# Kernel optimization log

Measured on AMD Instinct MI355X. Metric: run time of the kernel, lower is better.

The kernel has to match this reference:

```python
import jax, jax.numpy as jnp
import numpy as np

N_NODES = 100000
N_EDGES = 1600000
IN_DIM = 256
OUT_DIM = 128
SELF_LOOP_W = 2.0  # improved=True


def setup_inputs() -> dict:
    key = jax.random.key(0)
    ks = jax.random.split(key, 9)
    x = jax.random.normal(ks[0], (N_NODES, IN_DIM), dtype=jnp.float32)
    edge_index = jax.random.randint(ks[1], (2, N_EDGES), 0, N_NODES, dtype=jnp.int64)
    edge_weight = jax.random.uniform(ks[2], (N_EDGES,), dtype=jnp.float32)
    s1 = 1.0 / np.sqrt(IN_DIM)
    s2 = 1.0 / np.sqrt(OUT_DIM)
    W1 = jax.random.normal(ks[3], (IN_DIM, OUT_DIM), dtype=jnp.float32) * s1
    b1 = jnp.zeros((OUT_DIM,), dtype=jnp.float32)
    W_mu = jax.random.normal(ks[4], (OUT_DIM, OUT_DIM), dtype=jnp.float32) * s2
    b_mu = jnp.zeros((OUT_DIM,), dtype=jnp.float32)
    W_var = jax.random.normal(ks[5], (OUT_DIM, OUT_DIM), dtype=jnp.float32) * s2
    b_var = jnp.zeros((OUT_DIM,), dtype=jnp.float32)
    return {"x": x, "edge_index": edge_index, "edge_weight": edge_weight,
            "W1": W1, "b1": b1, "W_mu": W_mu, "b_mu": b_mu,
            "W_var": W_var, "b_var": b_var}


def _gcn_norm(edge_index, edge_weight, num_nodes):
    # add self loops with fill value 2.0 (improved=True), then symmetric norm
    loop = jnp.arange(num_nodes, dtype=edge_index.dtype)
    row = jnp.concatenate([edge_index[0], loop])
    col = jnp.concatenate([edge_index[1], loop])
    ew = jnp.concatenate([edge_weight,
                          jnp.full((num_nodes,), SELF_LOOP_W, dtype=edge_weight.dtype)])
    deg = jax.ops.segment_sum(ew, col, num_segments=num_nodes)
    dis = jnp.where(deg > 0, jax.lax.rsqrt(jnp.where(deg > 0, deg, 1.0)), 0.0)
    norm = dis[row] * ew * dis[col]
    return row, col, norm


def _gcn_conv(x, row, col, norm, W, b, num_nodes):
    xw = x @ W                      # [N, out]
    msg = xw[row] * norm[:, None]   # [E+N, out] per-edge messages
    out = jax.ops.segment_sum(msg, col, num_segments=num_nodes)
    return out + b


def reference(x, edge_index, edge_weight, W1, b1, W_mu, b_mu, W_var, b_var):
    n = x.shape[0]
    row, col, norm = _gcn_norm(edge_index, edge_weight, n)
    feat = jax.nn.relu(_gcn_conv(x, row, col, norm, W1, b1, n))
    mu = _gcn_conv(feat, row, col, norm, W_mu, b_mu, n)
    var = _gcn_conv(feat, row, col, norm, W_var, b_var, n)
    return (mu, var)
```

## Files before the change

### kernel.cpp

```cpp
#include <hip/hip_runtime.h>
#include <hip/hip_bf16.h>

#define CDIV(a,b) (((a)+(b)-1)/(b))

typedef __attribute__((ext_vector_type(8))) short short8;
typedef __attribute__((ext_vector_type(4))) float f32x4;

static __device__ inline short f2bf(float f) {
    union { __hip_bfloat16 h; short s; } u;
    u.h = __float2bfloat16(f);
    return u.s;
}
static __device__ inline ushort f2bfu(float f) { return (ushort)f2bf(f); }
static __device__ inline float bfu_lo(uint v) { return __uint_as_float(v << 16); }
static __device__ inline float bfu_hi(uint v) { return __uint_as_float(v & 0xffff0000u); }


__global__ __launch_bounds__(512) void k_init(unsigned long long* __restrict__ pack, int n,
                                              const float* __restrict__ W1,
                                              short* __restrict__ W1t,
                                              const float* __restrict__ Wmu,
                                              const float* __restrict__ Wvar,
                                              short* __restrict__ Wcat) {
    int i = blockIdx.x * 512 + threadIdx.x;
    if (i < n) pack[i] = 0ull;
    if (i < 128 * 256) {
        int k = i % 256, col = i / 256;
        W1t[i] = f2bf(W1[(size_t)k * 128 + col]);
    } else if (i < 2 * 128 * 256) {
        int j = i - 128 * 256;
        int k = j & 127, col = j >> 7;
        float v = (col < 128) ? Wmu[(size_t)k * 128 + col] : Wvar[(size_t)k * 128 + (col - 128)];
        Wcat[j] = f2bf(v);
    }
}


__global__ __launch_bounds__(512) void k_fat(const float* __restrict__ A,
                                             const short* __restrict__ Bt,
                                             ushort* __restrict__ C, int n, int nGB,
                                             const int* __restrict__ col,
                                             const float* __restrict__ ew,
                                             unsigned long long* __restrict__ pack,
                                             int* __restrict__ rank, int E) {
    const int K = 256;
    __shared__ short Blds[128 * K];
    int t = threadIdx.x;

    if (blockIdx.x >= nGB) {
        int e = (blockIdx.x - nGB) * 512 + t;
        if (e < E) {
            int c = col[e];
            unsigned long long q = (unsigned long long)(ew[e] * 16777216.0f + 0.5f);
            unsigned long long old = atomicAdd(&pack[c], (1ull << 40) | q);
            rank[e] = (int)(old >> 40);
        }
        return;
    }

    const int CHK = K / 8;
    for (int c = t; c < 128 * CHK; c += 512) {
        int colw = c / CHK;
        int kb  = (c % CHK) * 16;
        int dst = colw * (K * 2) + (kb ^ ((colw & 7) << 4));
        *(float4*)((char*)Blds + dst) =
            *(const float4*)((const char*)Bt + (size_t)colw * (K * 2) + kb);
    }
    __syncthreads();

    int wave = t >> 6, lane = t & 63;
    int lg = lane >> 4, lr = lane & 15;
    long row_base = (long)blockIdx.x * 256 + wave * 32;

    long ra0 = row_base + lr;      if (ra0 > n - 1) ra0 = n - 1;
    long ra1 = row_base + 16 + lr; if (ra1 > n - 1) ra1 = n - 1;

    f32x4 acc[2][8];
    #pragma unroll
    for (int i = 0; i < 2; ++i)
        #pragma unroll
        for (int j = 0; j < 8; ++j) acc[i][j] = (f32x4){0.f, 0.f, 0.f, 0.f};

    const float* pa0 = A + ra0 * K + lg * 8;
    const float* pa1 = A + ra1 * K + lg * 8;

    for (int k0 = 0; k0 < K; k0 += 32) {
        float4 x0 = *(const float4*)(pa0 + k0);
        float4 x1 = *(const float4*)(pa0 + k0 + 4);
        float4 y0 = *(const float4*)(pa1 + k0);
        float4 y1 = *(const float4*)(pa1 + k0 + 4);
        short8 a0, a1;
        a0[0]=f2bf(x0.x); a0[1]=f2bf(x0.y); a0[2]=f2bf(x0.z); a0[3]=f2bf(x0.w);
        a0[4]=f2bf(x1.x); a0[5]=f2bf(x1.y); a0[6]=f2bf(x1.z); a0[7]=f2bf(x1.w);
        a1[0]=f2bf(y0.x); a1[1]=f2bf(y0.y); a1[2]=f2bf(y0.z); a1[3]=f2bf(y0.w);
        a1[4]=f2bf(y1.x); a1[5]=f2bf(y1.y); a1[6]=f2bf(y1.z); a1[7]=f2bf(y1.w);

        int kb = (k0 + lg * 8) * 2;
        #pragma unroll
        for (int cb = 0; cb < 8; ++cb) {
            int colm = cb * 16 + lr;
            short8 b = *(short8*)((char*)Blds + colm * (K * 2) + (kb ^ ((colm & 7) << 4)));
            acc[0][cb] = __builtin_amdgcn_mfma_f32_16x16x32_bf16(a0, b, acc[0][cb], 0, 0, 0);
            acc[1][cb] = __builtin_amdgcn_mfma_f32_16x16x32_bf16(a1, b, acc[1][cb], 0, 0, 0);
        }
    }

    #pragma unroll
    for (int rf = 0; rf < 2; ++rf) {
        #pragma unroll
        for (int cb = 0; cb < 8; ++cb) {
            int colm = cb * 16 + lr;
            #pragma unroll
            for (int r = 0; r < 4; ++r) {
                long row = row_base + rf * 16 + lg * 4 + r;
                if (row < n) C[row * 128 + colm] = f2bfu(acc[rf][cb][r]);
            }
        }
    }
}


__global__ __launch_bounds__(256) void k_scan1(const unsigned long long* __restrict__ pack,
                                               float* __restrict__ dis,
                                               int* __restrict__ row_ptr,
                                               int* __restrict__ bsum, int n) {
    int t = threadIdx.x;
    int base = blockIdx.x * 1024 + t * 4;
    int v0 = 0, v1 = 0, v2 = 0, v3 = 0;
    #pragma unroll
    for (int j = 0; j < 4; ++j) {
        int idx = base + j;
        if (idx < n) {
            unsigned long long p = pack[idx];
            float deg = 2.0f + (float)(p & ((1ull << 40) - 1)) * (1.0f / 16777216.0f);
            dis[idx] = rsqrtf(deg);
            int c = (int)(p >> 40);
            if (j == 0) v0 = c; else if (j == 1) v1 = c; else if (j == 2) v2 = c; else v3 = c;
        }
    }
    int tsum = v0 + v1 + v2 + v3;
    int lane = t & 63, wv = t >> 6;
    int val = tsum;
    #pragma unroll
    for (int d = 1; d < 64; d <<= 1) {
        int u = __shfl_up(val, d, 64);
        if (lane >= d) val += u;
    }
    __shared__ int ws[4];
    if (lane == 63) ws[wv] = val;
    __syncthreads();
    int woff = 0;
    #pragma unroll
    for (int i = 0; i < 4; ++i) if (i < wv) woff += ws[i];
    int excl = woff + val - tsum;
    if (base + 0 < n) row_ptr[base + 0] = excl;  excl += v0;
    if (base + 1 < n) row_ptr[base + 1] = excl;  excl += v1;
    if (base + 2 < n) row_ptr[base + 2] = excl;  excl += v2;
    if (base + 3 < n) row_ptr[base + 3] = excl;
    if (t == 255) bsum[blockIdx.x] = woff + val;
}

__global__ __launch_bounds__(128) void k_scan2(int* bsum, int nb, int* row_ptr, int n, int E) {
    int t = threadIdx.x;
    int v = (t < nb) ? bsum[t] : 0;
    int lane = t & 63, wv = t >> 6;
    int val = v;
    #pragma unroll
    for (int d = 1; d < 64; d <<= 1) {
        int u = __shfl_up(val, d, 64);
        if (lane >= d) val += u;
    }
    __shared__ int ws[2];
    if (lane == 63) ws[wv] = val;
    __syncthreads();
    int woff = (wv == 1) ? ws[0] : 0;
    if (t < nb) bsum[t] = woff + val - v;
    if (t == 0) row_ptr[n] = E;
}

__global__ __launch_bounds__(256) void k_scan3(int* __restrict__ row_ptr,
                                               const int* __restrict__ bsum, int n) {
    int i = blockIdx.x * 256 + threadIdx.x;
    if (i < n) row_ptr[i] += bsum[i >> 10];
}

__global__ __launch_bounds__(512) void k_fill(const int* __restrict__ rowi,
                                              const int* __restrict__ coli,
                                              const float* __restrict__ ew,
                                              const int* __restrict__ rank,
                                              const float* __restrict__ dis,
                                              const int* __restrict__ row_ptr,
                                              int2* __restrict__ csr, int E) {
    int e = blockIdx.x * 512 + threadIdx.x;
    if (e < E) {
        int c = coli[e], r = rowi[e];
        int pos = row_ptr[c] + rank[e];
        csr[pos] = make_int2(r, __float_as_int(dis[r] * ew[e]));
    }
}


template<int OUTMODE>
__global__ __launch_bounds__(256) void k_agg(const uint* __restrict__ src,
                                             const int* __restrict__ row_ptr,
                                             const int2* __restrict__ csr,
                                             const float* __restrict__ dis,
                                             const float* __restrict__ bias,
                                             uint* __restrict__ dst, int n) {
    int wid = (blockIdx.x * 256 + threadIdx.x) >> 6;
    int lane = threadIdx.x & 63;
    if (wid >= n) return;
    int e0 = row_ptr[wid], e1 = row_ptr[wid + 1];

    float a0=0.f,b0=0.f,a1=0.f,b1=0.f,a2=0.f,b2=0.f,a3=0.f,b3=0.f;
    float a4=0.f,b4=0.f,a5=0.f,b5=0.f,a6=0.f,b6=0.f,a7=0.f,b7=0.f;
    int e = e0;
    for (; e + 7 < e1; e += 8) {
        int2 c0 = csr[e],     c1 = csr[e + 1], c2 = csr[e + 2], c3 = csr[e + 3];
        int2 c4 = csr[e + 4], c5 = csr[e + 5], c6 = csr[e + 6], c7 = csr[e + 7];
        uint v0 = src[(size_t)c0.x * 64 + lane];
        uint v1 = src[(size_t)c1.x * 64 + lane];
        uint v2 = src[(size_t)c2.x * 64 + lane];
        uint v3 = src[(size_t)c3.x * 64 + lane];
        uint v4 = src[(size_t)c4.x * 64 + lane];
        uint v5 = src[(size_t)c5.x * 64 + lane];
        uint v6 = src[(size_t)c6.x * 64 + lane];
        uint v7 = src[(size_t)c7.x * 64 + lane];
        float w0 = __int_as_float(c0.y), w1 = __int_as_float(c1.y);
        float w2 = __int_as_float(c2.y), w3 = __int_as_float(c3.y);
        float w4 = __int_as_float(c4.y), w5 = __int_as_float(c5.y);
        float w6 = __int_as_float(c6.y), w7 = __int_as_float(c7.y);
        a0 += w0 * bfu_lo(v0); b0 += w0 * bfu_hi(v0);
        a1 += w1 * bfu_lo(v1); b1 += w1 * bfu_hi(v1);
        a2 += w2 * bfu_lo(v2); b2 += w2 * bfu_hi(v2);
        a3 += w3 * bfu_lo(v3); b3 += w3 * bfu_hi(v3);
        a4 += w4 * bfu_lo(v4); b4 += w4 * bfu_hi(v4);
        a5 += w5 * bfu_lo(v5); b5 += w5 * bfu_hi(v5);
        a6 += w6 * bfu_lo(v6); b6 += w6 * bfu_hi(v6);
        a7 += w7 * bfu_lo(v7); b7 += w7 * bfu_hi(v7);
    }
    for (; e + 1 < e1; e += 2) {
        int2 c0 = csr[e], c1 = csr[e + 1];
        uint v0 = src[(size_t)c0.x * 64 + lane];
        uint v1 = src[(size_t)c1.x * 64 + lane];
        float w0 = __int_as_float(c0.y), w1 = __int_as_float(c1.y);
        a0 += w0 * bfu_lo(v0); b0 += w0 * bfu_hi(v0);
        a1 += w1 * bfu_lo(v1); b1 += w1 * bfu_hi(v1);
    }
    if (e < e1) {
        int2 c = csr[e];
        uint v = src[(size_t)c.x * 64 + lane];
        float w = __int_as_float(c.y);
        a0 += w * bfu_lo(v); b0 += w * bfu_hi(v);
    }
    float dc = dis[wid];
    uint sv = src[(size_t)wid * 64 + lane];
    float sw = 2.f * dc * dc;
    float ox = dc * (((a0 + a1) + (a2 + a3)) + ((a4 + a5) + (a6 + a7))) + sw * bfu_lo(sv);
    float oy = dc * (((b0 + b1) + (b2 + b3)) + ((b4 + b5) + (b6 + b7))) + sw * bfu_hi(sv);
    if constexpr (OUTMODE == 0) {
        ox += bias[lane * 2]; oy += bias[lane * 2 + 1];
        ox = fmaxf(ox, 0.f);  oy = fmaxf(oy, 0.f);
    }
    dst[(size_t)wid * 64 + lane] = (uint)f2bfu(ox) | ((uint)f2bfu(oy) << 16);
}


__global__ __launch_bounds__(512) void k_gemm2(const short* __restrict__ A,
                                               const short* __restrict__ Bt,
                                               const float* __restrict__ bmu,
                                               const float* __restrict__ bvar,
                                               float* __restrict__ out,
                                               int n) {
    const int K = 128;
    __shared__ short Blds[256 * K];
    int t = threadIdx.x;

    const int CHK = K / 8;
    for (int c = t; c < 256 * CHK; c += 512) {
        int col = c / CHK;
        int kb  = (c % CHK) * 16;
        int dst = col * (K * 2) + (kb ^ ((col & 7) << 4));
        *(float4*)((char*)Blds + dst) =
            *(const float4*)((const char*)Bt + (size_t)col * (K * 2) + kb);
    }
    __syncthreads();

    int wave = t >> 6, lane = t & 63;
    int lg = lane >> 4, lr = lane & 15;
    int colbase = (wave & 1) * 128;
    long row_base = (long)blockIdx.x * 128 + (wave >> 1) * 32;

    long ra0 = row_base + lr;      if (ra0 > n - 1) ra0 = n - 1;
    long ra1 = row_base + 16 + lr; if (ra1 > n - 1) ra1 = n - 1;

    f32x4 acc[2][8];
    #pragma unroll
    for (int i = 0; i < 2; ++i)
        #pragma unroll
        for (int j = 0; j < 8; ++j) acc[i][j] = (f32x4){0.f, 0.f, 0.f, 0.f};

    const short* pa0 = A + ra0 * K + lg * 8;
    const short* pa1 = A + ra1 * K + lg * 8;

    #pragma unroll
    for (int k0 = 0; k0 < K; k0 += 32) {
        short8 a0 = *(const short8*)(pa0 + k0);
        short8 a1 = *(const short8*)(pa1 + k0);
        int kb = (k0 + lg * 8) * 2;
        #pragma unroll
        for (int cb = 0; cb < 8; ++cb) {
            int col = colbase + cb * 16 + lr;
            short8 b = *(short8*)((char*)Blds + col * (K * 2) + (kb ^ ((col & 7) << 4)));
            acc[0][cb] = __builtin_amdgcn_mfma_f32_16x16x32_bf16(a0, b, acc[0][cb], 0, 0, 0);
            acc[1][cb] = __builtin_amdgcn_mfma_f32_16x16x32_bf16(a1, b, acc[1][cb], 0, 0, 0);
        }
    }

    #pragma unroll
    for (int rf = 0; rf < 2; ++rf) {
        #pragma unroll
        for (int cb = 0; cb < 8; ++cb) {
            int colc = colbase + cb * 16 + lr;
            bool is_var = colc >= 128;
            int col = is_var ? colc - 128 : colc;
            float bv = is_var ? bvar[col] : bmu[col];
            size_t obase = is_var ? (size_t)n * 128 : 0;
            #pragma unroll
            for (int r = 0; r < 4; ++r) {
                long row = row_base + rf * 16 + lg * 4 + r;
                if (row < n)
                    __builtin_nontemporal_store(acc[rf][cb][r] + bv,
                                                &out[obase + (size_t)row * 128 + col]);
            }
        }
    }
}


extern "C" void kernel_launch(void* const* d_in, const int* in_sizes, int n_in,
                              void* d_out, int out_size, void* d_ws, size_t ws_size,
                              hipStream_t stream) {
    const float* x    = (const float*)d_in[0];
    const int*   ei   = (const int*)d_in[1];
    const float* ew   = (const float*)d_in[2];
    const float* W1   = (const float*)d_in[3];
    const float* b1   = (const float*)d_in[4];
    const float* Wmu  = (const float*)d_in[5];
    const float* bmu  = (const float*)d_in[6];
    const float* Wvar = (const float*)d_in[7];
    const float* bvar = (const float*)d_in[8];

    const int E = in_sizes[2];
    const int N = in_sizes[0] / 256;
    const int* rowi = ei;
    const int* coli = ei + E;

    char* base = (char*)d_ws;
    size_t off = 0;
    auto alloc = [&](size_t bytes) -> void* {
        void* p = base + off;
        off = (off + bytes + 511) & ~(size_t)511;
        return p;
    };
    unsigned long long* pack = (unsigned long long*)alloc((size_t)N * 8);
    float* dis     = (float*)alloc((size_t)N * 4);
    int*   row_ptr = (int*)  alloc((size_t)(N + 1) * 4);
    int*   rank    = (int*)  alloc((size_t)E * 4);
    int*   bsum    = (int*)  alloc(1024 * 4);
    int2*  csr     = (int2*) alloc((size_t)E * 8);
    uint*  xw      = (uint*) alloc((size_t)N * 64 * 4);
    uint*  feat    = (uint*) alloc((size_t)N * 64 * 4);
    short* W1t     = (short*)alloc((size_t)256 * 128 * 2);
    short* Wcat    = (short*)alloc((size_t)256 * 128 * 2);
    uint*  g       = xw;

    int nb   = CDIV(N, 1024);
    int nGB  = CDIV(N, 256);
    int nCB  = CDIV(E, 512);

    k_init<<<CDIV(N, 512), 512, 0, stream>>>(pack, N, W1, W1t, Wmu, Wvar, Wcat);

    k_fat<<<nGB + nCB, 512, 0, stream>>>(x, W1t, (ushort*)xw, N, nGB, coli, ew, pack, rank, E);

    k_scan1<<<nb, 256, 0, stream>>>(pack, dis, row_ptr, bsum, N);
    k_scan2<<<1, 128, 0, stream>>>(bsum, nb, row_ptr, N, E);
    k_scan3<<<CDIV(N, 256), 256, 0, stream>>>(row_ptr, bsum, N);
    k_fill <<<CDIV(E, 512), 512, 0, stream>>>(rowi, coli, ew, rank, dis, row_ptr, csr, E);

    k_agg<0><<<CDIV(N * 64, 256), 256, 0, stream>>>(xw, row_ptr, csr, dis, b1, feat, N);
    k_agg<1><<<CDIV(N * 64, 256), 256, 0, stream>>>(feat, row_ptr, csr, dis, nullptr, g, N);
    k_gemm2<<<CDIV(N, 128), 512, 0, stream>>>((const short*)g, Wcat, bmu, bvar, (float*)d_out, N);
}
```

Before: 305.7 us.

## Halve k_fat LDS via two-phase K staging; split agg wave into edge halves

The first GEMM kernel now stages the 256-wide weight matrix in shared memory as two 128-wide halves. This halves its LDS footprint so more blocks can reside per CU, at the cost of an extra barrier and reload. The aggregation kernel now splits each wave into two 32-lane halves that each handle alternate edges with 8-byte vector loads of a full feature row. The halves are combined with a cross-half shuffle, which gives more gathers in flight per wave, and only half the lanes write the output.

```diff
diff --git a/kernel.cpp b/kernel.cpp
--- a/kernel.cpp
+++ b/kernel.cpp
@@ -43,8 +43,8 @@
                                              const float* __restrict__ ew,
                                              unsigned long long* __restrict__ pack,
                                              int* __restrict__ rank, int E) {
-    const int K = 256;
-    __shared__ short Blds[128 * K];
+    const int K = 256, KH = 128;
+    __shared__ short Blds[128 * KH];
     int t = threadIdx.x;
 
     if (blockIdx.x >= nGB) {
@@ -58,16 +58,6 @@
         return;
     }
 
-    const int CHK = K / 8;
-    for (int c = t; c < 128 * CHK; c += 512) {
-        int colw = c / CHK;
-        int kb  = (c % CHK) * 16;
-        int dst = colw * (K * 2) + (kb ^ ((colw & 7) << 4));
-        *(float4*)((char*)Blds + dst) =
-            *(const float4*)((const char*)Bt + (size_t)colw * (K * 2) + kb);
-    }
-    __syncthreads();
-
     int wave = t >> 6, lane = t & 63;
     int lg = lane >> 4, lr = lane & 15;
     long row_base = (long)blockIdx.x * 256 + wave * 32;
@@ -84,24 +74,39 @@
     const float* pa0 = A + ra0 * K + lg * 8;
     const float* pa1 = A + ra1 * K + lg * 8;
 
-    for (int k0 = 0; k0 < K; k0 += 32) {
-        float4 x0 = *(const float4*)(pa0 + k0);
-        float4 x1 = *(const float4*)(pa0 + k0 + 4);
-        float4 y0 = *(const float4*)(pa1 + k0);
-        float4 y1 = *(const float4*)(pa1 + k0 + 4);
-        short8 a0, a1;
-        a0[0]=f2bf(x0.x); a0[1]=f2bf(x0.y); a0[2]=f2bf(x0.z); a0[3]=f2bf(x0.w);
-        a0[4]=f2bf(x1.x); a0[5]=f2bf(x1.y); a0[6]=f2bf(x1.z); a0[7]=f2bf(x1.w);
-        a1[0]=f2bf(y0.x); a1[1]=f2bf(y0.y); a1[2]=f2bf(y0.z); a1[3]=f2bf(y0.w);
-        a1[4]=f2bf(y1.x); a1[5]=f2bf(y1.y); a1[6]=f2bf(y1.z); a1[7]=f2bf(y1.w);
-
-        int kb = (k0 + lg * 8) * 2;
-        #pragma unroll
-        for (int cb = 0; cb < 8; ++cb) {
-            int colm = cb * 16 + lr;
-            short8 b = *(short8*)((char*)Blds + colm * (K * 2) + (kb ^ ((colm & 7) << 4)));
-            acc[0][cb] = __builtin_amdgcn_mfma_f32_16x16x32_bf16(a0, b, acc[0][cb], 0, 0, 0);
-            acc[1][cb] = __builtin_amdgcn_mfma_f32_16x16x32_bf16(a1, b, acc[1][cb], 0, 0, 0);
+    #pragma unroll
+    for (int p = 0; p < 2; ++p) {
+        if (p) __syncthreads();
+        const int CHK = KH / 8;
+        for (int c = t; c < 128 * CHK; c += 512) {
+            int colw = c / CHK;
+            int kb  = (c % CHK) * 16;
+            int dst = colw * (KH * 2) + (kb ^ ((colw & 7) << 4));
+            *(float4*)((char*)Blds + dst) =
+                *(const float4*)((const char*)Bt + (size_t)colw * (K * 2) + p * (KH * 2) + kb);
+        }
+        __syncthreads();
+
+        for (int k0 = 0; k0 < KH; k0 += 32) {
+            int kg = p * KH + k0;
+            float4 x0 = *(const float4*)(pa0 + kg);
+            float4 x1 = *(const float4*)(pa0 + kg + 4);
+            float4 y0 = *(const float4*)(pa1 + kg);
+            float4 y1 = *(const float4*)(pa1 + kg + 4);
+            short8 a0, a1;
+            a0[0]=f2bf(x0.x); a0[1]=f2bf(x0.y); a0[2]=f2bf(x0.z); a0[3]=f2bf(x0.w);
+            a0[4]=f2bf(x1.x); a0[5]=f2bf(x1.y); a0[6]=f2bf(x1.z); a0[7]=f2bf(x1.w);
+            a1[0]=f2bf(y0.x); a1[1]=f2bf(y0.y); a1[2]=f2bf(y0.z); a1[3]=f2bf(y0.w);
+            a1[4]=f2bf(y1.x); a1[5]=f2bf(y1.y); a1[6]=f2bf(y1.z); a1[7]=f2bf(y1.w);
+
+            int kb = (k0 + lg * 8) * 2;
+            #pragma unroll
+            for (int cb = 0; cb < 8; ++cb) {
+                int colm = cb * 16 + lr;
+                short8 b = *(short8*)((char*)Blds + colm * (KH * 2) + (kb ^ ((colm & 7) << 4)));
+                acc[0][cb] = __builtin_amdgcn_mfma_f32_16x16x32_bf16(a0, b, acc[0][cb], 0, 0, 0);
+                acc[1][cb] = __builtin_amdgcn_mfma_f32_16x16x32_bf16(a1, b, acc[1][cb], 0, 0, 0);
+            }
         }
     }
 
@@ -201,68 +206,85 @@
 
 
 template<int OUTMODE>
-__global__ __launch_bounds__(256) void k_agg(const uint* __restrict__ src,
+__global__ __launch_bounds__(256) void k_agg(const uint2* __restrict__ src,
                                              const int* __restrict__ row_ptr,
                                              const int2* __restrict__ csr,
                                              const float* __restrict__ dis,
                                              const float* __restrict__ bias,
-                                             uint* __restrict__ dst, int n) {
+                                             uint2* __restrict__ dst, int n) {
     int wid = (blockIdx.x * 256 + threadIdx.x) >> 6;
     int lane = threadIdx.x & 63;
+    int hb = lane >> 5, lc = lane & 31;
     if (wid >= n) return;
     int e0 = row_ptr[wid], e1 = row_ptr[wid + 1];
 
-    float a0=0.f,b0=0.f,a1=0.f,b1=0.f,a2=0.f,b2=0.f,a3=0.f,b3=0.f;
-    float a4=0.f,b4=0.f,a5=0.f,b5=0.f,a6=0.f,b6=0.f,a7=0.f,b7=0.f;
+    float p00=0.f,p01=0.f,p02=0.f,p03=0.f;
+    float p10=0.f,p11=0.f,p12=0.f,p13=0.f;
+    float p20=0.f,p21=0.f,p22=0.f,p23=0.f;
+    float p30=0.f,p31=0.f,p32=0.f,p33=0.f;
+
     int e = e0;
     for (; e + 7 < e1; e += 8) {
-        int2 c0 = csr[e],     c1 = csr[e + 1], c2 = csr[e + 2], c3 = csr[e + 3];
-        int2 c4 = csr[e + 4], c5 = csr[e + 5], c6 = csr[e + 6], c7 = csr[e + 7];
-        uint v0 = src[(size_t)c0.x * 64 + lane];
-        uint v1 = src[(size_t)c1.x * 64 + lane];
-        uint v2 = src[(size_t)c2.x * 64 + lane];
-        uint v3 = src[(size_t)c3.x * 64 + lane];
-        uint v4 = src[(size_t)c4.x * 64 + lane];
-        uint v5 = src[(size_t)c5.x * 64 + lane];
-        uint v6 = src[(size_t)c6.x * 64 + lane];
-        uint v7 = src[(size_t)c7.x * 64 + lane];
+        int2 c0 = csr[e     + hb];
+        int2 c1 = csr[e + 2 + hb];
+        int2 c2 = csr[e + 4 + hb];
+        int2 c3 = csr[e + 6 + hb];
+        uint2 v0 = src[(size_t)c0.x * 32 + lc];
+        uint2 v1 = src[(size_t)c1.x * 32 + lc];
+        uint2 v2 = src[(size_t)c2.x * 32 + lc];
+        uint2 v3 = src[(size_t)c3.x * 32 + lc];
         float w0 = __int_as_float(c0.y), w1 = __int_as_float(c1.y);
         float w2 = __int_as_float(c2.y), w3 = __int_as_float(c3.y);
-        float w4 = __int_as_float(c4.y), w5 = __int_as_float(c5.y);
-        float w6 = __int_as_float(c6.y), w7 = __int_as_float(c7.y);
-        a0 += w0 * bfu_lo(v0); b0 += w0 * bfu_hi(v0);
-        a1 += w1 * bfu_lo(v1); b1 += w1 * bfu_hi(v1);
-        a2 += w2 * bfu_lo(v2); b2 += w2 * bfu_hi(v2);
-        a3 += w3 * bfu_lo(v3); b3 += w3 * bfu_hi(v3);
-        a4 += w4 * bfu_lo(v4); b4 += w4 * bfu_hi(v4);
-        a5 += w5 * bfu_lo(v5); b5 += w5 * bfu_hi(v5);
-        a6 += w6 * bfu_lo(v6); b6 += w6 * bfu_hi(v6);
-        a7 += w7 * bfu_lo(v7); b7 += w7 * bfu_hi(v7);
+        p00 += w0 * bfu_lo(v0.x); p01 += w0 * bfu_hi(v0.x);
+        p02 += w0 * bfu_lo(v0.y); p03 += w0 * bfu_hi(v0.y);
+        p10 += w1 * bfu_lo(v1.x); p11 += w1 * bfu_hi(v1.x);
+        p12 += w1 * bfu_lo(v1.y); p13 += w1 * bfu_hi(v1.y);
+        p20 += w2 * bfu_lo(v2.x); p21 += w2 * bfu_hi(v2.x);
+        p22 += w2 * bfu_lo(v2.y); p23 += w2 * bfu_hi(v2.y);
+        p30 += w3 * bfu_lo(v3.x); p31 += w3 * bfu_hi(v3.x);
+        p32 += w3 * bfu_lo(v3.y); p33 += w3 * bfu_hi(v3.y);
     }
     for (; e + 1 < e1; e += 2) {
-        int2 c0 = csr[e], c1 = csr[e + 1];
-        uint v0 = src[(size_t)c0.x * 64 + lane];
-        uint v1 = src[(size_t)c1.x * 64 + lane];
-        float w0 = __int_as_float(c0.y), w1 = __int_as_float(c1.y);
-        a0 += w0 * bfu_lo(v0); b0 += w0 * bfu_hi(v0);
-        a1 += w1 * bfu_lo(v1); b1 += w1 * bfu_hi(v1);
-    }
-    if (e < e1) {
+        int2 c = csr[e + hb];
+        uint2 v = src[(size_t)c.x * 32 + lc];
+        float w = __int_as_float(c.y);
+        p00 += w * bfu_lo(v.x); p01 += w * bfu_hi(v.x);
+        p02 += w * bfu_lo(v.y); p03 += w * bfu_hi(v.y);
+    }
+    if (e < e1 && hb == 0) {
         int2 c = csr[e];
-        uint v = src[(size_t)c.x * 64 + lane];
+        uint2 v = src[(size_t)c.x * 32 + lc];
         float w = __int_as_float(c.y);
-        a0 += w * bfu_lo(v); b0 += w * bfu_hi(v);
-    }
+        p10 += w * bfu_lo(v.x); p11 += w * bfu_hi(v.x);
+        p12 += w * bfu_lo(v.y); p13 += w * bfu_hi(v.y);
+    }
+
+    float x0 = (p00 + p10) + (p20 + p30);
+    float x1 = (p01 + p11) + (p21 + p31);
+    float x2 = (p02 + p12) + (p22 + p32);
+    float x3 = (p03 + p13) + (p23 + p33);
+    x0 = x0 + __shfl_xor(x0, 32);
+    x1 = x1 + __shfl_xor(x1, 32);
+    x2 = x2 + __shfl_xor(x2, 32);
+    x3 = x3 + __shfl_xor(x3, 32);
+
     float dc = dis[wid];
-    uint sv = src[(size_t)wid * 64 + lane];
+    uint2 sv = src[(size_t)wid * 32 + lc];
     float sw = 2.f * dc * dc;
-    float ox = dc * (((a0 + a1) + (a2 + a3)) + ((a4 + a5) + (a6 + a7))) + sw * bfu_lo(sv);
-    float oy = dc * (((b0 + b1) + (b2 + b3)) + ((b4 + b5) + (b6 + b7))) + sw * bfu_hi(sv);
+    float o0 = dc * x0 + sw * bfu_lo(sv.x);
+    float o1 = dc * x1 + sw * bfu_hi(sv.x);
+    float o2 = dc * x2 + sw * bfu_lo(sv.y);
+    float o3 = dc * x3 + sw * bfu_hi(sv.y);
     if constexpr (OUTMODE == 0) {
-        ox += bias[lane * 2]; oy += bias[lane * 2 + 1];
-        ox = fmaxf(ox, 0.f);  oy = fmaxf(oy, 0.f);
-    }
-    dst[(size_t)wid * 64 + lane] = (uint)f2bfu(ox) | ((uint)f2bfu(oy) << 16);
+        float4 bv = *(const float4*)(bias + lc * 4);
+        o0 += bv.x; o1 += bv.y; o2 += bv.z; o3 += bv.w;
+        o0 = fmaxf(o0, 0.f); o1 = fmaxf(o1, 0.f);
+        o2 = fmaxf(o2, 0.f); o3 = fmaxf(o3, 0.f);
+    }
+    if (hb == 0)
+        dst[(size_t)wid * 32 + lc] =
+            make_uint2((uint)f2bfu(o0) | ((uint)f2bfu(o1) << 16),
+                       (uint)f2bfu(o2) | ((uint)f2bfu(o3) << 16));
 }
 
 
@@ -388,7 +410,7 @@
     k_scan3<<<CDIV(N, 256), 256, 0, stream>>>(row_ptr, bsum, N);
     k_fill <<<CDIV(E, 512), 512, 0, stream>>>(rowi, coli, ew, rank, dis, row_ptr, csr, E);
 
-    k_agg<0><<<CDIV(N * 64, 256), 256, 0, stream>>>(xw, row_ptr, csr, dis, b1, feat, N);
-    k_agg<1><<<CDIV(N * 64, 256), 256, 0, stream>>>(feat, row_ptr, csr, dis, nullptr, g, N);
+    k_agg<0><<<CDIV(N * 64, 256), 256, 0, stream>>>((const uint2*)xw, row_ptr, csr, dis, b1, (uint2*)feat, N);
+    k_agg<1><<<CDIV(N * 64, 256), 256, 0, stream>>>((const uint2*)feat, row_ptr, csr, dis, nullptr, (uint2*)g, N);
     k_gemm2<<<CDIV(N, 128), 512, 0, stream>>>((const short*)g, Wcat, bmu, bvar, (float*)d_out, N);
 }
```

Result: no change. 307.1 us (+0.5%).
